# Performance work log

Measured on AMD Instinct MI355X. Metric: run time of the kernel, lower is better.

## Reference

```python
import jax, jax.numpy as jnp
import numpy as np

DIM = 96
WS = 16            # window_size
OVERLAP = 0.5
UPSCALE = 2
NH = 1             # num_heads
OWIN = int(WS * OVERLAP) + WS          # 24, overlap_win_size
WSU = UPSCALE * WS                     # 32, window_size_up
TABLE = (WSU + OWIN - 1) ** 2          # 3025
PAD = (OWIN - WS) // 2                 # 4


def compute_rpi():
    # Faithful to calculate_rpi_owxra (incl. torch negative-index wraparound -> modulo).
    wsu, cur = WSU, WS + int(OVERLAP * WS)
    a = np.arange(wsu)
    coords_up = np.stack(np.meshgrid(a, a, indexing='ij')).reshape(2, -1)      # (2, wsu^2)
    b = np.arange(cur)
    coords_cur = np.stack(np.meshgrid(b, b, indexing='ij')).reshape(2, -1)     # (2, cur^2)
    rel = coords_cur[:, None, :] - coords_up[:, :, None]                       # (2, wsu^2, cur^2)
    rel = rel.transpose(1, 2, 0).astype(np.int64)
    rel += wsu - cur + 1
    rel[:, :, 0] *= wsu + cur - 1
    idx = rel.sum(-1) % TABLE                                                  # (wsu^2, cur^2)
    return jnp.asarray(idx)


def setup_inputs() -> dict:
    key = jax.random.key(0)
    ks = jax.random.split(key, 6)
    x = jax.random.normal(ks[0], (2, 128, 128, DIM), dtype=jnp.float32)
    x2 = jax.random.normal(ks[1], (128, WSU * WSU, DIM), dtype=jnp.float32)  # (b*nw, 1024, 96)
    Wkv = jax.random.normal(ks[2], (DIM, 2 * DIM), dtype=jnp.float32) * 0.02
    bkv = jnp.zeros((2 * DIM,), dtype=jnp.float32)
    bias_table = jax.random.normal(ks[3], (TABLE, NH), dtype=jnp.float32) * 0.02
    Wproj = jax.random.normal(ks[4], (DIM, DIM), dtype=jnp.float32) * 0.02
    bproj = jnp.zeros((DIM,), dtype=jnp.float32)
    return {"x": x, "x2": x2, "Wkv": Wkv, "bkv": bkv,
            "bias_table": bias_table, "Wproj": Wproj, "bproj": bproj}


def _forward(x, x2, Wkv, bkv, bias_table, Wproj, bproj, rpi):
    b, h, w, c = x.shape
    d = c // NH
    scale = d ** (-0.5)
    kv = x @ Wkv + bkv                                        # (b,h,w,2c); cols [:c]=k, [c:]=v
    p = jnp.pad(kv, ((0, 0), (PAD, PAD), (PAD, PAD), (0, 0)))
    nwh, nww = h // WS, w // WS
    idx_h = (jnp.arange(nwh) * WS)[:, None] + jnp.arange(OWIN)  # (nwh, OWIN)
    idx_w = (jnp.arange(nww) * WS)[:, None] + jnp.arange(OWIN)
    rows = p[:, idx_h]                                        # (b,nwh,OWIN,W',2c)
    wins = rows[:, :, :, idx_w]                               # (b,nwh,OWIN,nww,OWIN,2c)
    wins = wins.transpose(0, 1, 3, 2, 4, 5).reshape(b * nwh * nww, OWIN * OWIN, 2 * c)
    k = wins[..., :c]
    v = wins[..., c:]
    nwb, Q, _ = x2.shape
    K = OWIN * OWIN
    q = x2.reshape(nwb, Q, NH, d).transpose(0, 2, 1, 3) * scale   # (nwb,nh,Q,d)
    kh = k.reshape(nwb, K, NH, d).transpose(0, 2, 1, 3)
    vh = v.reshape(nwb, K, NH, d).transpose(0, 2, 1, 3)
    attn = jnp.einsum('bhqd,bhkd->bhqk', q, kh)
    bias = bias_table[rpi].transpose(2, 0, 1)                  # (nh,Q,K)
    attn = jax.nn.softmax(attn + bias[None], axis=-1)
    out = jnp.einsum('bhqk,bhkd->bhqd', attn, vh)
    out = out.transpose(0, 2, 1, 3).reshape(nwb, Q, c)
    return out @ Wproj + bproj


def reference(x, x2, Wkv, bkv, bias_table, Wproj, bproj):
    rpi = compute_rpi()
    return _forward(x, x2, Wkv, bkv, bias_table, Wproj, bproj, rpi)
```

## Files before the change

### kernel.cpp

```cpp
#include <hip/hip_runtime.h>
#include <hip/hip_bf16.h>
#include <stdint.h>

#define QLEN 1024
#define KLEN 576
#define TABLE_SZ 3025

typedef __attribute__((ext_vector_type(8))) short short8;
typedef __attribute__((ext_vector_type(4))) float floatx4;
typedef __attribute__((ext_vector_type(16))) float floatx16;
typedef __attribute__((ext_vector_type(4))) unsigned short ushort4v;
typedef __attribute__((ext_vector_type(2))) int int2v;

static __device__ __forceinline__ unsigned short f2b(float f) {
    union { float f; unsigned int u; } v; v.f = f;
    return (unsigned short)((v.u + 0x7FFFu + ((v.u >> 16) & 1u)) >> 16);
}
static __device__ __forceinline__ int pk2(float lo, float hi) {
    union { __hip_bfloat162 h; int i; } u;
    u.h = __float22bfloat162_rn(float2{lo, hi});
    return u.i;
}
union W8 { unsigned int u[4]; short8 s8; };

static __device__ __forceinline__ short8 bfrag(int w0, int w1, int w2, int w3) {
    int2v pa = __builtin_amdgcn_permlane32_swap(w0, w2, false, false);
    int2v pb = __builtin_amdgcn_permlane32_swap(w1, w3, false, false);
    W8 w;
    w.u[0] = (unsigned)pa[0];
    w.u[1] = (unsigned)pb[0];
    w.u[2] = (unsigned)pa[1];
    w.u[3] = (unsigned)pb[1];
    return w.s8;
}

__global__ void prep_kernel(const float* __restrict__ Wkv, const float* __restrict__ Wproj,
                            const float* __restrict__ table,
                            unsigned short* __restrict__ WkvT, unsigned short* __restrict__ WprojT,
                            float* __restrict__ biasM) {
    const float LOG2E = 1.4426950408889634f;
    int t0 = blockIdx.x * blockDim.x + threadIdx.x;
    int stride = gridDim.x * blockDim.x;
    for (int i = t0; i < QLEN * KLEN; i += stride) {
        int qi = i / KLEN, kk = i - qi * KLEN;
        int rel0 = kk / 24 - qi / 32 + 9;
        int rel1 = kk % 24 - qi % 32 + 9;
        int s = rel0 * 55 + rel1;
        if (s < 0) s += TABLE_SZ;
        biasM[i] = table[s] * LOG2E;
    }
    for (int i = t0; i < 192 * 96; i += stride) {
        int n = i / 96, k = i - n * 96;
        WkvT[i] = f2b(Wkv[k * 192 + n]);
    }
    for (int i = t0; i < 96 * 96; i += stride) {
        int j = i / 96, d = i - j * 96;
        WprojT[i] = f2b(Wproj[d * 96 + j]);
    }
}

__global__ __launch_bounds__(256) void kv_kernel(const float* __restrict__ x,
        const unsigned short* __restrict__ WkvT, const float* __restrict__ bkv,
        unsigned short* __restrict__ Kpad, unsigned short* __restrict__ Vpad) {
    __shared__ unsigned short xt[64 * 104];
    __shared__ unsigned short vt2[96 * 72];
    int tid = threadIdx.x;
    int mbase = blockIdx.x * 64;
    int bb = mbase >> 14, rem = mbase & 16383;
    int hy = rem >> 7, hx0 = rem & 127;
    #pragma unroll
    for (int it = 0; it < 6; ++it) {
        int c = tid + it * 256;
        int row = c / 24, col4 = (c - row * 24) * 4;
        floatx4 v = *(const floatx4*)(x + (mbase + row) * 96 + col4);
        ushort4v o;
        o[0] = f2b(v[0]); o[1] = f2b(v[1]); o[2] = f2b(v[2]); o[3] = f2b(v[3]);
        *(ushort4v*)&xt[row * 104 + col4] = o;
    }
    __syncthreads();
    int lane = tid & 63, wv = tid >> 6;
    int g = lane >> 4, c16 = lane & 15;
    short8 a[3];
    #pragma unroll
    for (int c = 0; c < 3; ++c)
        a[c] = *(const short8*)&xt[(wv * 16 + c16) * 104 + c * 32 + g * 8];
    floatx4 acc[12];
    #pragma unroll
    for (int nt = 0; nt < 12; ++nt) acc[nt] = (floatx4){0.f, 0.f, 0.f, 0.f};
    #pragma unroll
    for (int nt = 0; nt < 12; ++nt)
        #pragma unroll
        for (int c = 0; c < 3; ++c) {
            short8 b = *(const short8*)(WkvT + (nt * 16 + c16) * 96 + c * 32 + g * 8);
            acc[nt] = __builtin_amdgcn_mfma_f32_16x16x32_bf16(a[c], b, acc[nt], 0, 0, 0);
        }
    #pragma unroll
    for (int nt = 0; nt < 6; ++nt) {
        int col = nt * 16 + c16;
        float bk = bkv[col];
        #pragma unroll
        for (int r = 0; r < 4; ++r) {
            int rowl = wv * 16 + g * 4 + r;
            Kpad[((bb * 136 + hy + 4) * 136 + hx0 + rowl + 4) * 96 + col] = f2b(acc[nt][r] + bk);
        }
    }
    #pragma unroll
    for (int nt = 6; nt < 12; ++nt) {
        int d = nt * 16 + c16 - 96;
        float bk = bkv[96 + d];
        #pragma unroll
        for (int r = 0; r < 4; ++r) {
            int rowl = wv * 16 + g * 4 + r;
            vt2[d * 72 + rowl] = f2b(acc[nt][r] + bk);
        }
    }
    __syncthreads();
    #pragma unroll
    for (int it = 0; it < 3; ++it) {
        int v = tid + it * 256;
        int d = v >> 3, ch = v & 7;
        short8 val = *(const short8*)&vt2[d * 72 + ch * 8];
        *(short8*)(Vpad + ((bb * 96 + d) * 136 + hy + 4) * 136 + hx0 + 4 + ch * 8) = val;
    }
}

__global__ __launch_bounds__(256, 3) void attn_kernel(const float* __restrict__ x2,
        const unsigned short* __restrict__ Kpad, const unsigned short* __restrict__ Vpad,
        const float* __restrict__ biasM,
        const unsigned short* __restrict__ WprojT, const float* __restrict__ bproj,
        float* __restrict__ out) {
    __shared__ unsigned short Kt[64 * 104];
    __shared__ unsigned short Vt[96 * 72];

    int bid_hw = blockIdx.x;
    int bid = (bid_hw & 7) * 128 + (bid_hw >> 3);
    int wb = bid >> 3, qb = bid & 7;
    int bb = wb >> 6, wy = (wb >> 3) & 7, wx = wb & 7;
    int tid = threadIdx.x, lane = tid & 63, wv = tid >> 6;
    int l31 = lane & 31, h = lane >> 5;
    int qlo = qb * 128 + wv * 32;

    const float qscale = 0.10206207261596577f * 1.4426950408889634f;
    short8 qf[6];
    #pragma unroll
    for (int c = 0; c < 6; ++c) {
        const float* src = x2 + (wb * 1024 + qlo + l31) * 96 + c * 16 + h * 8;
        floatx4 v0 = *(const floatx4*)src;
        floatx4 v1 = *(const floatx4*)(src + 4);
        short8 q;
        #pragma unroll
        for (int i = 0; i < 4; ++i) {
            q[i]     = (short)f2b(v0[i] * qscale);
            q[4 + i] = (short)f2b(v1[i] * qscale);
        }
        qf[c] = q;
    }

    short8 pre[6];
    auto loadpre = [&](int kt) {
        #pragma unroll
        for (int it = 0; it < 6; ++it) {
            int c = tid + it * 256;
            if (c < 768) {
                int kr = c / 12, part = c - kr * 12;
                int kk = kt * 64 + kr;
                int oh = kk / 24, ow = kk - oh * 24;
                pre[it] = *(const short8*)(Kpad + ((bb * 136 + wy * 16 + oh) * 136 + wx * 16 + ow) * 96 + part * 8);
            } else {
                int v = c - 768;
                int d = v >> 3, ch = v & 7;
                int kk0 = kt * 64 + ch * 8;
                int oh = kk0 / 24, ow0 = kk0 - oh * 24;
                pre[it] = *(const short8*)(Vpad + ((bb * 96 + d) * 136 + wy * 16 + oh) * 136 + wx * 16 + ow0);
            }
        }
    };

    floatx16 Oa[3];
    #pragma unroll
    for (int dt = 0; dt < 3; ++dt)
        Oa[dt] = (floatx16){0.f,0.f,0.f,0.f,0.f,0.f,0.f,0.f,0.f,0.f,0.f,0.f,0.f,0.f,0.f,0.f};
    float lp = 0.f;

    loadpre(0);
    for (int kt = 0; kt < 9; ++kt) {
        __syncthreads();
        #pragma unroll
        for (int it = 0; it < 6; ++it) {
            int c = tid + it * 256;
            if (c < 768) {
                int kr = c / 12, part = c - kr * 12;
                *(short8*)&Kt[kr * 104 + part * 8] = pre[it];
            } else {
                int v = c - 768;
                int d = v >> 3, ch = v & 7;
                *(short8*)&Vt[d * 72 + ch * 8] = pre[it];
            }
        }
        if (kt < 8) loadpre(kt + 1);
        __syncthreads();

        const float* brow = biasM + (qlo + l31) * 576 + kt * 64 + h * 4;
        #pragma unroll
        for (int half = 0; half < 2; ++half) {
            floatx16 s = (floatx16){0.f,0.f,0.f,0.f,0.f,0.f,0.f,0.f,0.f,0.f,0.f,0.f,0.f,0.f,0.f,0.f};
            __builtin_amdgcn_s_setprio(1);
            #pragma unroll
            for (int c = 0; c < 6; ++c) {
                short8 kf = *(const short8*)&Kt[(half * 32 + l31) * 104 + c * 16 + h * 8];
                s = __builtin_amdgcn_mfma_f32_32x32x16_bf16(kf, qf[c], s, 0, 0, 0);
            }
            __builtin_amdgcn_s_setprio(0);
            int w[8];
            #pragma unroll
            for (int t = 0; t < 4; ++t) {
                floatx4 bv = *(const floatx4*)(brow + half * 32 + t * 8);
                float p0 = __builtin_amdgcn_exp2f(s[4 * t + 0] + bv[0]);
                float p1 = __builtin_amdgcn_exp2f(s[4 * t + 1] + bv[1]);
                float p2 = __builtin_amdgcn_exp2f(s[4 * t + 2] + bv[2]);
                float p3 = __builtin_amdgcn_exp2f(s[4 * t + 3] + bv[3]);
                lp += (p0 + p1) + (p2 + p3);
                w[t * 2 + 0] = pk2(p0, p1);
                w[t * 2 + 1] = pk2(p2, p3);
            }
            #pragma unroll
            for (int kc = 0; kc < 2; ++kc) {
                short8 pf = bfrag(w[kc * 4 + 0], w[kc * 4 + 1], w[kc * 4 + 2], w[kc * 4 + 3]);
                __builtin_amdgcn_s_setprio(1);
                #pragma unroll
                for (int dt = 0; dt < 3; ++dt) {
                    short8 vf = *(const short8*)&Vt[(dt * 32 + l31) * 72 + (half * 2 + kc) * 16 + h * 8];
                    Oa[dt] = __builtin_amdgcn_mfma_f32_32x32x16_bf16(vf, pf, Oa[dt], 0, 0, 0);
                }
                __builtin_amdgcn_s_setprio(0);
            }
        }
    }

    lp += __shfl_xor(lp, 32);
    float inv = 1.0f / lp;
    short8 of[6];
    #pragma unroll
    for (int dt = 0; dt < 3; ++dt) {
        int ow[8];
        #pragma unroll
        for (int t = 0; t < 4; ++t) {
            ow[t * 2 + 0] = pk2(Oa[dt][4 * t + 0] * inv, Oa[dt][4 * t + 1] * inv);
            ow[t * 2 + 1] = pk2(Oa[dt][4 * t + 2] * inv, Oa[dt][4 * t + 3] * inv);
        }
        of[dt * 2 + 0] = bfrag(ow[0], ow[1], ow[2], ow[3]);
        of[dt * 2 + 1] = bfrag(ow[4], ow[5], ow[6], ow[7]);
    }
    #pragma unroll
    for (int jt = 0; jt < 3; ++jt) {
        floatx16 acc = (floatx16){0.f,0.f,0.f,0.f,0.f,0.f,0.f,0.f,0.f,0.f,0.f,0.f,0.f,0.f,0.f,0.f};
        #pragma unroll
        for (int st = 0; st < 6; ++st) {
            short8 wf = *(const short8*)(WprojT + (jt * 32 + l31) * 96 + st * 16 + h * 8);
            acc = __builtin_amdgcn_mfma_f32_32x32x16_bf16(wf, of[st], acc, 0, 0, 0);
        }
        int row = wb * 1024 + qlo + l31;
        #pragma unroll
        for (int t = 0; t < 4; ++t) {
            floatx4 bp = *(const floatx4*)(bproj + jt * 32 + t * 8 + h * 4);
            #pragma unroll
            for (int r = 0; r < 4; ++r)
                out[row * 96 + jt * 32 + t * 8 + h * 4 + r] = acc[4 * t + r] + bp[r];
        }
    }
}

extern "C" void kernel_launch(void* const* d_in, const int* in_sizes, int n_in,
                              void* d_out, int out_size, void* d_ws, size_t ws_size,
                              hipStream_t stream) {
    const float* x     = (const float*)d_in[0];
    const float* x2    = (const float*)d_in[1];
    const float* Wkv   = (const float*)d_in[2];
    const float* bkv   = (const float*)d_in[3];
    const float* table = (const float*)d_in[4];
    const float* Wproj = (const float*)d_in[5];
    const float* bproj = (const float*)d_in[6];
    float* out = (float*)d_out;

    char* ws = (char*)d_ws;
    unsigned short* Kpad   = (unsigned short*)ws;
    unsigned short* Vpad   = (unsigned short*)(ws + 7102464);
    float*          biasM  = (float*)(ws + 14204928);
    unsigned short* WkvT   = (unsigned short*)(ws + 16564224);
    unsigned short* WprojT = (unsigned short*)(ws + 16601088);

    hipMemsetAsync(ws, 0, 14204928, stream);
    hipLaunchKernelGGL(prep_kernel, dim3(512), dim3(256), 0, stream,
                       Wkv, Wproj, table, WkvT, WprojT, biasM);
    hipLaunchKernelGGL(kv_kernel, dim3(512), dim3(256), 0, stream,
                       x, WkvT, bkv, Kpad, Vpad);
    hipLaunchKernelGGL(attn_kernel, dim3(1024), dim3(256), 0, stream,
                       x2, Kpad, Vpad, biasM, WprojT, bproj, out);
}
```

Baseline: 111.0 us.

## Read K/V MFMA fragments directly from global memory instead of LDS staging

Removes the shared-memory K and V tiles, the register prefetch pipeline and both per-tile barriers. Each wave now loads its K and V MFMA operands straight from the padded global K/V buffers, computing window offsets per lane. This avoids LDS traffic and synchronisation, but every wave re-reads the same K/V data through L1/L2 with no software prefetch, so memory latency sits directly in front of each MFMA.

```diff
diff --git a/kernel.cpp b/kernel.cpp
--- a/kernel.cpp
+++ b/kernel.cpp
@@ -129,9 +129,6 @@
         const float* __restrict__ biasM,
         const unsigned short* __restrict__ WprojT, const float* __restrict__ bproj,
         float* __restrict__ out) {
-    __shared__ unsigned short Kt[64 * 104];
-    __shared__ unsigned short Vt[96 * 72];
-
     int bid_hw = blockIdx.x;
     int bid = (bid_hw & 7) * 128 + (bid_hw >> 3);
     int wb = bid >> 3, qb = bid & 7;
@@ -156,25 +153,8 @@
         qf[c] = q;
     }
 
-    short8 pre[6];
-    auto loadpre = [&](int kt) {
-        #pragma unroll
-        for (int it = 0; it < 6; ++it) {
-            int c = tid + it * 256;
-            if (c < 768) {
-                int kr = c / 12, part = c - kr * 12;
-                int kk = kt * 64 + kr;
-                int oh = kk / 24, ow = kk - oh * 24;
-                pre[it] = *(const short8*)(Kpad + ((bb * 136 + wy * 16 + oh) * 136 + wx * 16 + ow) * 96 + part * 8);
-            } else {
-                int v = c - 768;
-                int d = v >> 3, ch = v & 7;
-                int kk0 = kt * 64 + ch * 8;
-                int oh = kk0 / 24, ow0 = kk0 - oh * 24;
-                pre[it] = *(const short8*)(Vpad + ((bb * 96 + d) * 136 + wy * 16 + oh) * 136 + wx * 16 + ow0);
-            }
-        }
-    };
+    const unsigned short* Kbase = Kpad + (size_t)((bb * 136 + wy * 16) * 136 + wx * 16) * 96 + h * 8;
+    const unsigned short* Vbase = Vpad + (size_t)(bb * 96) * 18496 + (wy * 16) * 136 + wx * 16;
 
     floatx16 Oa[3];
     #pragma unroll
@@ -182,32 +162,18 @@
         Oa[dt] = (floatx16){0.f,0.f,0.f,0.f,0.f,0.f,0.f,0.f,0.f,0.f,0.f,0.f,0.f,0.f,0.f,0.f};
     float lp = 0.f;
 
-    loadpre(0);
     for (int kt = 0; kt < 9; ++kt) {
-        __syncthreads();
-        #pragma unroll
-        for (int it = 0; it < 6; ++it) {
-            int c = tid + it * 256;
-            if (c < 768) {
-                int kr = c / 12, part = c - kr * 12;
-                *(short8*)&Kt[kr * 104 + part * 8] = pre[it];
-            } else {
-                int v = c - 768;
-                int d = v >> 3, ch = v & 7;
-                *(short8*)&Vt[d * 72 + ch * 8] = pre[it];
-            }
-        }
-        if (kt < 8) loadpre(kt + 1);
-        __syncthreads();
-
         const float* brow = biasM + (qlo + l31) * 576 + kt * 64 + h * 4;
         #pragma unroll
         for (int half = 0; half < 2; ++half) {
+            int kk = kt * 64 + half * 32 + l31;
+            int oh = kk / 24, ow = kk - oh * 24;
+            const unsigned short* krow = Kbase + (oh * 136 + ow) * 96;
             floatx16 s = (floatx16){0.f,0.f,0.f,0.f,0.f,0.f,0.f,0.f,0.f,0.f,0.f,0.f,0.f,0.f,0.f,0.f};
             __builtin_amdgcn_s_setprio(1);
             #pragma unroll
             for (int c = 0; c < 6; ++c) {
-                short8 kf = *(const short8*)&Kt[(half * 32 + l31) * 104 + c * 16 + h * 8];
+                short8 kf = *(const short8*)(krow + c * 16);
                 s = __builtin_amdgcn_mfma_f32_32x32x16_bf16(kf, qf[c], s, 0, 0, 0);
             }
             __builtin_amdgcn_s_setprio(0);
@@ -226,10 +192,13 @@
             #pragma unroll
             for (int kc = 0; kc < 2; ++kc) {
                 short8 pf = bfrag(w[kc * 4 + 0], w[kc * 4 + 1], w[kc * 4 + 2], w[kc * 4 + 3]);
+                int kk0 = kt * 64 + (half * 2 + kc) * 16 + h * 8;
+                int ohv = kk0 / 24, owv = kk0 - ohv * 24;
+                const unsigned short* vcol = Vbase + ohv * 136 + owv;
                 __builtin_amdgcn_s_setprio(1);
                 #pragma unroll
                 for (int dt = 0; dt < 3; ++dt) {
-                    short8 vf = *(const short8*)&Vt[(dt * 32 + l31) * 72 + (half * 2 + kc) * 16 + h * 8];
+                    short8 vf = *(const short8*)(vcol + (size_t)(dt * 32 + l31) * 18496);
                     Oa[dt] = __builtin_amdgcn_mfma_f32_32x32x16_bf16(vf, pf, Oa[dt], 0, 0, 0);
                 }
                 __builtin_amdgcn_s_setprio(0);
```

Result: slower. 161.9 us (+45.8%).
